# Kernel optimization log

Measured on AMD Instinct MI355X. Metric: run time of the kernel, lower is better.

The kernel has to match this reference:

```python
import jax, jax.numpy as jnp
import numpy as np

D_MODEL = 1024
NUM_HEADS = 16
D_HEAD = D_MODEL // NUM_HEADS


def setup_inputs() -> dict:
    key = jax.random.key(0)
    ks = jax.random.split(key, 9)
    B, L, E = 2, 2048, D_MODEL
    bound = 1.0 / np.sqrt(E)  # torch nn.Linear init range
    inp = {
        "query": jax.random.normal(ks[0], (B, L, E), dtype=jnp.float32),
        "key": jax.random.normal(ks[1], (B, L, E), dtype=jnp.float32),
        "value": jax.random.normal(ks[2], (B, L, E), dtype=jnp.float32),
        "wq": jax.random.uniform(ks[3], (E, E), jnp.float32, -bound, bound),
        "bq": jax.random.uniform(ks[4], (E,), jnp.float32, -bound, bound),
        "wk": jax.random.uniform(ks[5], (E, E), jnp.float32, -bound, bound),
        "bk": jax.random.uniform(ks[6], (E,), jnp.float32, -bound, bound),
        "wv": jax.random.uniform(ks[7], (E, E), jnp.float32, -bound, bound),
        "bv": jax.random.uniform(ks[8], (E,), jnp.float32, -bound, bound),
    }
    return inp


def reference(query, key, value, wq, bq, wk, bk, wv, bv):
    B, L, E = query.shape
    H, Dh = NUM_HEADS, D_HEAD
    scale = Dh ** 0.5
    # linear projections (torch Linear: x @ W.T + b)
    q = (query @ wq.T + bq).reshape(B, L, H, Dh).transpose(0, 2, 1, 3)  # bhld
    k = (key @ wk.T + bk).reshape(B, L, H, Dh).transpose(0, 2, 1, 3)
    v = (value @ wv.T + bv).reshape(B, L, H, Dh).transpose(0, 2, 1, 3)
    scores = jnp.einsum("bhld,bhsd->bhls", q, k) / scale
    attn = jax.nn.softmax(scores, axis=-1)  # dropout p=0 / eval: identity
    out = jnp.einsum("bhls,bhsd->bhld", attn, v)
    return out.transpose(0, 2, 1, 3).reshape(B, L, E)
```

## Files before the change

### kernel.cpp

```cpp
#include <hip/hip_runtime.h>
#include <hip/hip_bf16.h>


typedef __attribute__((ext_vector_type(8))) short short8;
typedef __attribute__((ext_vector_type(4))) short short4v;
typedef __attribute__((ext_vector_type(4))) float floatx4;

#define L_SEQ 2048
#define EMB 1024
#define NH 16
#define DH 64
#define QSCALE 0.18033688011112042f

__device__ __forceinline__ void gl16(const void* g, void* l) {
  __builtin_amdgcn_global_load_lds(
      (const __attribute__((address_space(1))) void*)g,
      (__attribute__((address_space(3))) void*)l, 16, 0, 0);
}

__global__ void cvt6_kernel(const float* __restrict__ s0, const float* __restrict__ s1,
                            const float* __restrict__ s2, const float* __restrict__ s3,
                            const float* __restrict__ s4, const float* __restrict__ s5,
                            __hip_bfloat16* __restrict__ d0, __hip_bfloat16* __restrict__ d1,
                            __hip_bfloat16* __restrict__ d2, __hip_bfloat16* __restrict__ d3,
                            __hip_bfloat16* __restrict__ d4, __hip_bfloat16* __restrict__ d5,
                            int nx8, int nw8) {
  const int t = blockIdx.y;
  const float* src = (t == 0) ? s0 : (t == 1) ? s1 : (t == 2) ? s2
                   : (t == 3) ? s3 : (t == 4) ? s4 : s5;
  __hip_bfloat16* dst = (t == 0) ? d0 : (t == 1) ? d1 : (t == 2) ? d2
                      : (t == 3) ? d3 : (t == 4) ? d4 : d5;
  const int n8 = (t < 3) ? nx8 : nw8;
  int i = blockIdx.x * blockDim.x + threadIdx.x;
  const int stride = gridDim.x * blockDim.x;
  for (; i < n8; i += stride) {
    const float4* s4p = (const float4*)src;
    float4 a = s4p[2 * i];
    float4 b = s4p[2 * i + 1];
    union { short8 v; __hip_bfloat16 h[8]; } u;
    u.h[0] = __float2bfloat16(a.x); u.h[1] = __float2bfloat16(a.y);
    u.h[2] = __float2bfloat16(a.z); u.h[3] = __float2bfloat16(a.w);
    u.h[4] = __float2bfloat16(b.x); u.h[5] = __float2bfloat16(b.y);
    u.h[6] = __float2bfloat16(b.z); u.h[7] = __float2bfloat16(b.w);
    *(short8*)(dst + 8 * i) = u.v;
  }
}

__global__ __launch_bounds__(256) void proj_kernel(
    const __hip_bfloat16* __restrict__ xq, const __hip_bfloat16* __restrict__ xk,
    const __hip_bfloat16* __restrict__ xv,
    const __hip_bfloat16* __restrict__ wqb, const __hip_bfloat16* __restrict__ wkb,
    const __hip_bfloat16* __restrict__ wvb,
    const float* __restrict__ bq, const float* __restrict__ bk,
    const float* __restrict__ bv,
    __hip_bfloat16* __restrict__ Qb, __hip_bfloat16* __restrict__ Kb,
    __hip_bfloat16* __restrict__ Vt) {
  __shared__ __hip_bfloat16 lds[2 * 128 * 64];
  const int tid = threadIdx.x;
  const int bx = blockIdx.x;
  const int by = blockIdx.y;
  const int p = by >> 3;
  const int n0 = (by & 7) * 128;
  const int m0 = bx * 128;
  const __hip_bfloat16* X = (p == 0) ? xq : (p == 1) ? xk : xv;
  const __hip_bfloat16* W = (p == 0) ? wqb : (p == 1) ? wkb : wvb;
  const float* bias = (p == 0) ? bq : (p == 1) ? bk : bv;

  const int w = tid >> 6, ln = tid & 63;
  const int wm = w & 1, wn = w >> 1;
  const int quad = ln >> 4, lr = ln & 15;

  floatx4 acc[4][4];
#pragma unroll
  for (int i = 0; i < 4; ++i)
#pragma unroll
    for (int j = 0; j < 4; ++j) acc[i][j] = (floatx4){0.f, 0.f, 0.f, 0.f};

  const int srow = tid >> 3;
  const int scol = (tid & 7) * 8;

  for (int kt = 0; kt < 16; ++kt) {
    const int k0 = kt * 64;
#pragma unroll
    for (int i = 0; i < 4; ++i) {
      gl16(X + (size_t)(m0 + i * 32 + srow) * EMB + k0 + scol,
           lds + i * 2048 + tid * 8);
      gl16(W + (size_t)(n0 + i * 32 + srow) * EMB + k0 + scol,
           lds + 8192 + i * 2048 + tid * 8);
    }
    __syncthreads();
#pragma unroll
    for (int ks = 0; ks < 2; ++ks) {
      short8 af[4], bf[4];
#pragma unroll
      for (int mt = 0; mt < 4; ++mt)
        af[mt] = *(const short8*)(lds + (wm * 64 + mt * 16 + lr) * 64 + ks * 32 + quad * 8);
#pragma unroll
      for (int nt = 0; nt < 4; ++nt)
        bf[nt] = *(const short8*)(lds + 8192 + (wn * 64 + nt * 16 + lr) * 64 + ks * 32 + quad * 8);
#pragma unroll
      for (int mt = 0; mt < 4; ++mt)
#pragma unroll
        for (int nt = 0; nt < 4; ++nt)
          acc[mt][nt] = __builtin_amdgcn_mfma_f32_16x16x32_bf16(
              af[mt], bf[nt], acc[mt][nt], 0, 0, 0);
    }
    __syncthreads();
  }

#pragma unroll
  for (int mt = 0; mt < 4; ++mt) {
#pragma unroll
    for (int nt = 0; nt < 4; ++nt) {
      const int ng = n0 + wn * 64 + nt * 16 + lr;
      const int h = ng >> 6, d = ng & 63;
      const int mbase = m0 + wm * 64 + mt * 16 + quad * 4;
      const float bb = bias[ng];
      if (p == 2) {
        union { short4v v; __hip_bfloat16 h4[4]; } u;
#pragma unroll
        for (int r = 0; r < 4; ++r) u.h4[r] = __float2bfloat16(acc[mt][nt][r] + bb);
        const int b = mbase >> 11, lq = mbase & 2047;
        *(short4v*)(Vt + ((size_t)((b * NH + h) * DH + d)) * L_SEQ + lq) = u.v;
      } else {
        __hip_bfloat16* dst = (p == 0) ? Qb : Kb;
        const float scl = (p == 0) ? QSCALE : 1.0f;
#pragma unroll
        for (int r = 0; r < 4; ++r) {
          const int m = mbase + r;
          const int b = m >> 11, lq = m & 2047;
          dst[((size_t)((b * NH + h) * L_SEQ + lq)) * DH + d] =
              __float2bfloat16((acc[mt][nt][r] + bb) * scl);
        }
      }
    }
  }
}

__global__ __launch_bounds__(256, 4) void attn_kernel(
    const __hip_bfloat16* __restrict__ Qb, const __hip_bfloat16* __restrict__ Kb,
    const __hip_bfloat16* __restrict__ Vt, float* __restrict__ out) {
  __shared__ __align__(16) __hip_bfloat16 Kl[2][64 * 64];
  __shared__ __align__(16) __hip_bfloat16 Vl[2][64 * 64];
  __shared__ __align__(16) __hip_bfloat16 Pl[4][16 * 64];

  const int tid = threadIdx.x;
  const int w = tid >> 6, ln = tid & 63;
  const int quad = ln >> 4, lr = ln & 15;
  const int bh = blockIdx.y;
  const int q0 = blockIdx.x * 64;
  const __hip_bfloat16* Qp = Qb + (size_t)bh * L_SEQ * DH;
  const __hip_bfloat16* Kp = Kb + (size_t)bh * L_SEQ * DH;
  const __hip_bfloat16* Vp = Vt + (size_t)bh * DH * L_SEQ;

  short8 qf[2];
#pragma unroll
  for (int kk = 0; kk < 2; ++kk)
    qf[kk] = *(const short8*)(Qp + (size_t)(q0 + w * 16 + lr) * DH + kk * 32 + quad * 8);

  int koff[2], voff[2], loff[2];
#pragma unroll
  for (int i = 0; i < 2; ++i) {
    const int idx = i * 256 + tid;
    const int srow = idx >> 3;
    const int c = (idx & 7) ^ (srow & 7);
    koff[i] = srow * DH + c * 8;
    voff[i] = srow * L_SEQ + c * 8;
    loff[i] = idx * 8;
  }

  floatx4 acc[4];
  float psum[4];
#pragma unroll
  for (int nt = 0; nt < 4; ++nt) acc[nt] = (floatx4){0.f, 0.f, 0.f, 0.f};
#pragma unroll
  for (int r = 0; r < 4; ++r) psum[r] = 0.f;

  {
    const int s0 = 0;
#pragma unroll
    for (int i = 0; i < 2; ++i) gl16(Kp + (size_t)s0 * DH + koff[i], &Kl[0][loff[i]]);
#pragma unroll
    for (int i = 0; i < 2; ++i) gl16(Vp + s0 + voff[i], &Vl[0][loff[i]]);
  }

  const int xsw = lr & 7;

  for (int it = 0; it < 32; ++it) {
    __syncthreads();
    if (it + 1 < 32) {
      const int s0 = (it + 1) * 64;
      const int bf = (it + 1) & 1;
#pragma unroll
      for (int i = 0; i < 2; ++i) gl16(Kp + (size_t)s0 * DH + koff[i], &Kl[bf][loff[i]]);
#pragma unroll
      for (int i = 0; i < 2; ++i) gl16(Vp + s0 + voff[i], &Vl[bf][loff[i]]);
    }
    const __hip_bfloat16* Kt = Kl[it & 1];
    const __hip_bfloat16* Vtile = Vl[it & 1];

    floatx4 sc[4];
#pragma unroll
    for (int nt = 0; nt < 4; ++nt) sc[nt] = (floatx4){0.f, 0.f, 0.f, 0.f};
#pragma unroll
    for (int kk = 0; kk < 2; ++kk) {
      short8 kf[4];
#pragma unroll
      for (int nt = 0; nt < 4; ++nt)
        kf[nt] = *(const short8*)(Kt + ((nt * 16 + lr) * 8 + ((kk * 4 + quad) ^ xsw)) * 8);
#pragma unroll
      for (int nt = 0; nt < 4; ++nt)
        sc[nt] = __builtin_amdgcn_mfma_f32_16x16x32_bf16(qf[kk], kf[nt], sc[nt], 0, 0, 0);
    }

#pragma unroll
    for (int nt = 0; nt < 4; ++nt)
#pragma unroll
      for (int r = 0; r < 4; ++r) {
        const float pv = __builtin_amdgcn_exp2f(sc[nt][r]);
        sc[nt][r] = pv;
        psum[r] += pv;
      }

#pragma unroll
    for (int nt = 0; nt < 4; ++nt) {
      const int cb = nt * 2 + (lr >> 3);
#pragma unroll
      for (int r = 0; r < 4; ++r) {
        const int row = quad * 4 + r;
        Pl[w][row * 64 + ((cb ^ (row & 7)) * 8) + (lr & 7)] = __float2bfloat16(sc[nt][r]);
      }
    }

#pragma unroll
    for (int kk = 0; kk < 2; ++kk) {
      short8 pf = *(const short8*)(Pl[w] + (lr * 8 + ((kk * 4 + quad) ^ xsw)) * 8);
      short8 vf[4];
#pragma unroll
      for (int nt = 0; nt < 4; ++nt)
        vf[nt] = *(const short8*)(Vtile + ((nt * 16 + lr) * 8 + ((kk * 4 + quad) ^ xsw)) * 8);
#pragma unroll
      for (int nt = 0; nt < 4; ++nt)
        acc[nt] = __builtin_amdgcn_mfma_f32_16x16x32_bf16(pf, vf[nt], acc[nt], 0, 0, 0);
    }
  }

#pragma unroll
  for (int msk = 1; msk < 16; msk <<= 1)
#pragma unroll
    for (int r = 0; r < 4; ++r) psum[r] += __shfl_xor(psum[r], msk, 64);

  const int b = bh >> 4, h = bh & 15;
#pragma unroll
  for (int r = 0; r < 4; ++r) {
    const float inv = 1.0f / psum[r];
    const int lq = q0 + w * 16 + quad * 4 + r;
#pragma unroll
    for (int nt = 0; nt < 4; ++nt)
      out[((size_t)(b * L_SEQ + lq)) * EMB + h * DH + nt * 16 + lr] = acc[nt][r] * inv;
  }
}

extern "C" void kernel_launch(void* const* d_in, const int* in_sizes, int n_in,
                              void* d_out, int out_size, void* d_ws, size_t ws_size,
                              hipStream_t stream) {
  const float* xq = (const float*)d_in[0];
  const float* xk = (const float*)d_in[1];
  const float* xv = (const float*)d_in[2];
  const float* wq = (const float*)d_in[3];
  const float* bq = (const float*)d_in[4];
  const float* wk = (const float*)d_in[5];
  const float* bk = (const float*)d_in[6];
  const float* wv = (const float*)d_in[7];
  const float* bv = (const float*)d_in[8];

  const size_t NX = (size_t)4096 * 1024;
  const size_t NW = (size_t)1024 * 1024;
  __hip_bfloat16* xbq = (__hip_bfloat16*)d_ws;
  __hip_bfloat16* xbk = xbq + NX;
  __hip_bfloat16* xbv = xbk + NX;
  __hip_bfloat16* wbq = xbv + NX;
  __hip_bfloat16* wbk = wbq + NW;
  __hip_bfloat16* wbv = wbk + NW;
  __hip_bfloat16* Qb = wbv + NW;
  __hip_bfloat16* Kb = Qb + NX;
  __hip_bfloat16* Vt = Kb + NX;

  cvt6_kernel<<<dim3(1024, 6), 256, 0, stream>>>(xq, xk, xv, wq, wk, wv,
                                                 xbq, xbk, xbv, wbq, wbk, wbv,
                                                 (int)(NX / 8), (int)(NW / 8));

  proj_kernel<<<dim3(32, 24), 256, 0, stream>>>(xbq, xbk, xbv, wbq, wbk, wbv,
                                                bq, bk, bv, Qb, Kb, Vt);
  attn_kernel<<<dim3(32, 32), 256, 0, stream>>>(Qb, Kb, Vt, (float*)d_out);
}
```

Measured before the change: 206.4 us.

## Stage projection epilogue through LDS and enlarge attention per-wave query tile

The projection epilogue now writes its results into a padded LDS tile and then issues coalesced 16-byte row stores to Q, K and transposed V, replacing scattered 2-byte and strided global stores. The attention kernel now gives each wave 64 query rows instead of 16, using 128-thread blocks, so each K/V fragment loaded from LDS is reused across four query sub-tiles. S is computed as K·Q^T so that P can be written to LDS in packed 4-element stores. The exchange is much higher register pressure (a 64-float accumulator per lane) and fewer blocks (512), which may lower occupancy.

```diff
diff --git a/kernel.cpp b/kernel.cpp
--- a/kernel.cpp
+++ b/kernel.cpp
@@ -46,6 +46,7 @@
   }
 }
 
+#define CPAD 136
 __global__ __launch_bounds__(256) void proj_kernel(
     const __hip_bfloat16* __restrict__ xq, const __hip_bfloat16* __restrict__ xk,
     const __hip_bfloat16* __restrict__ xv,
@@ -55,7 +56,7 @@
     const float* __restrict__ bv,
     __hip_bfloat16* __restrict__ Qb, __hip_bfloat16* __restrict__ Kb,
     __hip_bfloat16* __restrict__ Vt) {
-  __shared__ __hip_bfloat16 lds[2 * 128 * 64];
+  __shared__ __align__(16) __hip_bfloat16 lds[128 * CPAD];
   const int tid = threadIdx.x;
   const int bx = blockIdx.x;
   const int by = blockIdx.y;
@@ -108,60 +109,83 @@
     __syncthreads();
   }
 
-#pragma unroll
-  for (int mt = 0; mt < 4; ++mt) {
+  if (p == 2) {
 #pragma unroll
     for (int nt = 0; nt < 4; ++nt) {
-      const int ng = n0 + wn * 64 + nt * 16 + lr;
+      const int nl = wn * 64 + nt * 16 + lr;
+      const float bb = bias[n0 + nl];
+#pragma unroll
+      for (int mt = 0; mt < 4; ++mt) {
+        union { short4v v; __hip_bfloat16 h4[4]; } u;
+#pragma unroll
+        for (int r = 0; r < 4; ++r) u.h4[r] = __float2bfloat16(acc[mt][nt][r] + bb);
+        *(short4v*)(&lds[nl * CPAD + wm * 64 + mt * 16 + quad * 4]) = u.v;
+      }
+    }
+  } else {
+    const float scl = (p == 0) ? QSCALE : 1.0f;
+#pragma unroll
+    for (int nt = 0; nt < 4; ++nt) {
+      const int nl = wn * 64 + nt * 16 + lr;
+      const float bb = bias[n0 + nl];
+#pragma unroll
+      for (int mt = 0; mt < 4; ++mt)
+#pragma unroll
+        for (int r = 0; r < 4; ++r)
+          lds[(wm * 64 + mt * 16 + quad * 4 + r) * CPAD + nl] =
+              __float2bfloat16((acc[mt][nt][r] + bb) * scl);
+    }
+  }
+  __syncthreads();
+
+  {
+    const int tr = tid >> 1, half = tid & 1;
+    const int b = m0 >> 11;
+    const __hip_bfloat16* src = lds + tr * CPAD + half * 64;
+    __hip_bfloat16* g;
+    if (p == 2) {
+      const int ng = n0 + tr;
       const int h = ng >> 6, d = ng & 63;
-      const int mbase = m0 + wm * 64 + mt * 16 + quad * 4;
-      const float bb = bias[ng];
-      if (p == 2) {
-        union { short4v v; __hip_bfloat16 h4[4]; } u;
-#pragma unroll
-        for (int r = 0; r < 4; ++r) u.h4[r] = __float2bfloat16(acc[mt][nt][r] + bb);
-        const int b = mbase >> 11, lq = mbase & 2047;
-        *(short4v*)(Vt + ((size_t)((b * NH + h) * DH + d)) * L_SEQ + lq) = u.v;
-      } else {
-        __hip_bfloat16* dst = (p == 0) ? Qb : Kb;
-        const float scl = (p == 0) ? QSCALE : 1.0f;
-#pragma unroll
-        for (int r = 0; r < 4; ++r) {
-          const int m = mbase + r;
-          const int b = m >> 11, lq = m & 2047;
-          dst[((size_t)((b * NH + h) * L_SEQ + lq)) * DH + d] =
-              __float2bfloat16((acc[mt][nt][r] + bb) * scl);
-        }
-      }
-    }
-  }
-}
-
-__global__ __launch_bounds__(256, 4) void attn_kernel(
+      g = Vt + ((size_t)((b * NH + h) * DH + d)) * L_SEQ + (m0 & 2047) + half * 64;
+    } else {
+      __hip_bfloat16* dst = (p == 0) ? Qb : Kb;
+      const int m = m0 + tr;
+      const int h = (n0 >> 6) + half;
+      g = dst + ((size_t)((b * NH + h) * L_SEQ + (m & 2047))) * DH;
+    }
+#pragma unroll
+    for (int j = 0; j < 8; ++j)
+      *(short8*)(g + j * 8) = *(const short8*)(src + j * 8);
+  }
+}
+
+__global__ __launch_bounds__(128, 2) void attn_kernel(
     const __hip_bfloat16* __restrict__ Qb, const __hip_bfloat16* __restrict__ Kb,
     const __hip_bfloat16* __restrict__ Vt, float* __restrict__ out) {
-  __shared__ __align__(16) __hip_bfloat16 Kl[2][64 * 64];
-  __shared__ __align__(16) __hip_bfloat16 Vl[2][64 * 64];
-  __shared__ __align__(16) __hip_bfloat16 Pl[4][16 * 64];
+  __shared__ __align__(16) __hip_bfloat16 Kl[2][4096];
+  __shared__ __align__(16) __hip_bfloat16 Vl[2][4096];
+  __shared__ __align__(16) __hip_bfloat16 Pl[2][4096];
 
   const int tid = threadIdx.x;
   const int w = tid >> 6, ln = tid & 63;
   const int quad = ln >> 4, lr = ln & 15;
   const int bh = blockIdx.y;
-  const int q0 = blockIdx.x * 64;
+  const int q0 = blockIdx.x * 128 + w * 64;
   const __hip_bfloat16* Qp = Qb + (size_t)bh * L_SEQ * DH;
   const __hip_bfloat16* Kp = Kb + (size_t)bh * L_SEQ * DH;
   const __hip_bfloat16* Vp = Vt + (size_t)bh * DH * L_SEQ;
 
-  short8 qf[2];
-#pragma unroll
-  for (int kk = 0; kk < 2; ++kk)
-    qf[kk] = *(const short8*)(Qp + (size_t)(q0 + w * 16 + lr) * DH + kk * 32 + quad * 8);
-
-  int koff[2], voff[2], loff[2];
-#pragma unroll
-  for (int i = 0; i < 2; ++i) {
-    const int idx = i * 256 + tid;
+  short8 qf[4][2];
+#pragma unroll
+  for (int qs = 0; qs < 4; ++qs)
+#pragma unroll
+    for (int kk = 0; kk < 2; ++kk)
+      qf[qs][kk] = *(const short8*)(Qp + (size_t)(q0 + qs * 16 + lr) * DH + kk * 32 + quad * 8);
+
+  int koff[4], voff[4], loff[4];
+#pragma unroll
+  for (int i = 0; i < 4; ++i) {
+    const int idx = i * 128 + tid;
     const int srow = idx >> 3;
     const int c = (idx & 7) ^ (srow & 7);
     koff[i] = srow * DH + c * 8;
@@ -169,20 +193,19 @@
     loff[i] = idx * 8;
   }
 
-  floatx4 acc[4];
+  floatx4 acc[4][4];
   float psum[4];
 #pragma unroll
-  for (int nt = 0; nt < 4; ++nt) acc[nt] = (floatx4){0.f, 0.f, 0.f, 0.f};
-#pragma unroll
-  for (int r = 0; r < 4; ++r) psum[r] = 0.f;
-
-  {
-    const int s0 = 0;
-#pragma unroll
-    for (int i = 0; i < 2; ++i) gl16(Kp + (size_t)s0 * DH + koff[i], &Kl[0][loff[i]]);
-#pragma unroll
-    for (int i = 0; i < 2; ++i) gl16(Vp + s0 + voff[i], &Vl[0][loff[i]]);
-  }
+  for (int qs = 0; qs < 4; ++qs) {
+    psum[qs] = 0.f;
+#pragma unroll
+    for (int nt = 0; nt < 4; ++nt) acc[qs][nt] = (floatx4){0.f, 0.f, 0.f, 0.f};
+  }
+
+#pragma unroll
+  for (int i = 0; i < 4; ++i) gl16(Kp + koff[i], &Kl[0][loff[i]]);
+#pragma unroll
+  for (int i = 0; i < 4; ++i) gl16(Vp + voff[i], &Vl[0][loff[i]]);
 
   const int xsw = lr & 7;
 
@@ -192,72 +215,73 @@
       const int s0 = (it + 1) * 64;
       const int bf = (it + 1) & 1;
 #pragma unroll
-      for (int i = 0; i < 2; ++i) gl16(Kp + (size_t)s0 * DH + koff[i], &Kl[bf][loff[i]]);
-#pragma unroll
-      for (int i = 0; i < 2; ++i) gl16(Vp + s0 + voff[i], &Vl[bf][loff[i]]);
+      for (int i = 0; i < 4; ++i) gl16(Kp + (size_t)s0 * DH + koff[i], &Kl[bf][loff[i]]);
+#pragma unroll
+      for (int i = 0; i < 4; ++i) gl16(Vp + s0 + voff[i], &Vl[bf][loff[i]]);
     }
     const __hip_bfloat16* Kt = Kl[it & 1];
     const __hip_bfloat16* Vtile = Vl[it & 1];
 
-    floatx4 sc[4];
-#pragma unroll
-    for (int nt = 0; nt < 4; ++nt) sc[nt] = (floatx4){0.f, 0.f, 0.f, 0.f};
+#pragma unroll
+    for (int mt = 0; mt < 4; ++mt) {
+      floatx4 sc[4];
+#pragma unroll
+      for (int qs = 0; qs < 4; ++qs) sc[qs] = (floatx4){0.f, 0.f, 0.f, 0.f};
+#pragma unroll
+      for (int kk = 0; kk < 2; ++kk) {
+        const short8 kf = *(const short8*)(Kt + ((mt * 16 + lr) * 8 + ((kk * 4 + quad) ^ xsw)) * 8);
+#pragma unroll
+        for (int qs = 0; qs < 4; ++qs)
+          sc[qs] = __builtin_amdgcn_mfma_f32_16x16x32_bf16(kf, qf[qs][kk], sc[qs], 0, 0, 0);
+      }
+      const int cch = mt * 2 + (quad >> 1);
+#pragma unroll
+      for (int qs = 0; qs < 4; ++qs) {
+        union { short4v v; __hip_bfloat16 h4[4]; } u;
+#pragma unroll
+        for (int r = 0; r < 4; ++r) {
+          const float pv = __builtin_amdgcn_exp2f(sc[qs][r]);
+          psum[qs] += pv;
+          u.h4[r] = __float2bfloat16(pv);
+        }
+        const int row = qs * 16 + lr;
+        *(short4v*)(&Pl[w][row * 64 + ((cch ^ xsw) * 8 + (quad & 1) * 4)]) = u.v;
+      }
+    }
+
 #pragma unroll
     for (int kk = 0; kk < 2; ++kk) {
-      short8 kf[4];
-#pragma unroll
-      for (int nt = 0; nt < 4; ++nt)
-        kf[nt] = *(const short8*)(Kt + ((nt * 16 + lr) * 8 + ((kk * 4 + quad) ^ xsw)) * 8);
-#pragma unroll
-      for (int nt = 0; nt < 4; ++nt)
-        sc[nt] = __builtin_amdgcn_mfma_f32_16x16x32_bf16(qf[kk], kf[nt], sc[nt], 0, 0, 0);
-    }
-
-#pragma unroll
-    for (int nt = 0; nt < 4; ++nt)
-#pragma unroll
-      for (int r = 0; r < 4; ++r) {
-        const float pv = __builtin_amdgcn_exp2f(sc[nt][r]);
-        sc[nt][r] = pv;
-        psum[r] += pv;
-      }
-
-#pragma unroll
-    for (int nt = 0; nt < 4; ++nt) {
-      const int cb = nt * 2 + (lr >> 3);
-#pragma unroll
-      for (int r = 0; r < 4; ++r) {
-        const int row = quad * 4 + r;
-        Pl[w][row * 64 + ((cb ^ (row & 7)) * 8) + (lr & 7)] = __float2bfloat16(sc[nt][r]);
-      }
-    }
-
-#pragma unroll
-    for (int kk = 0; kk < 2; ++kk) {
-      short8 pf = *(const short8*)(Pl[w] + (lr * 8 + ((kk * 4 + quad) ^ xsw)) * 8);
       short8 vf[4];
 #pragma unroll
       for (int nt = 0; nt < 4; ++nt)
         vf[nt] = *(const short8*)(Vtile + ((nt * 16 + lr) * 8 + ((kk * 4 + quad) ^ xsw)) * 8);
 #pragma unroll
+      for (int qs = 0; qs < 4; ++qs) {
+        const short8 pf = *(const short8*)(&Pl[w][(qs * 16 + lr) * 64 + ((kk * 4 + quad) ^ xsw) * 8]);
+#pragma unroll
+        for (int nt = 0; nt < 4; ++nt)
+          acc[qs][nt] = __builtin_amdgcn_mfma_f32_16x16x32_bf16(pf, vf[nt], acc[qs][nt], 0, 0, 0);
+      }
+    }
+  }
+
+#pragma unroll
+  for (int qs = 0; qs < 4; ++qs) {
+    psum[qs] += __shfl_xor(psum[qs], 16, 64);
+    psum[qs] += __shfl_xor(psum[qs], 32, 64);
+  }
+
+  const int b = bh >> 4, h = bh & 15;
+#pragma unroll
+  for (int qs = 0; qs < 4; ++qs) {
+#pragma unroll
+    for (int r = 0; r < 4; ++r) {
+      const float inv = 1.0f / __shfl(psum[qs], quad * 4 + r, 64);
+      const int lq = q0 + qs * 16 + quad * 4 + r;
+#pragma unroll
       for (int nt = 0; nt < 4; ++nt)
-        acc[nt] = __builtin_amdgcn_mfma_f32_16x16x32_bf16(pf, vf[nt], acc[nt], 0, 0, 0);
-    }
-  }
-
-#pragma unroll
-  for (int msk = 1; msk < 16; msk <<= 1)
-#pragma unroll
-    for (int r = 0; r < 4; ++r) psum[r] += __shfl_xor(psum[r], msk, 64);
-
-  const int b = bh >> 4, h = bh & 15;
-#pragma unroll
-  for (int r = 0; r < 4; ++r) {
-    const float inv = 1.0f / psum[r];
-    const int lq = q0 + w * 16 + quad * 4 + r;
-#pragma unroll
-    for (int nt = 0; nt < 4; ++nt)
-      out[((size_t)(b * L_SEQ + lq)) * EMB + h * DH + nt * 16 + lr] = acc[nt][r] * inv;
+        out[((size_t)(b * L_SEQ + lq)) * EMB + h * DH + nt * 16 + lr] = acc[qs][nt][r] * inv;
+    }
   }
 }
 
@@ -292,5 +316,5 @@
 
   proj_kernel<<<dim3(32, 24), 256, 0, stream>>>(xbq, xbk, xbv, wbq, wbk, wbv,
                                                 bq, bk, bv, Qb, Kb, Vt);
-  attn_kernel<<<dim3(32, 32), 256, 0, stream>>>(Qb, Kb, Vt, (float*)d_out);
-}
+  attn_kernel<<<dim3(16, 32), 128, 0, stream>>>(Qb, Kb, Vt, (float*)d_out);
+}
```

After: 229.6 us. +11.3%, slower.
